# Optimization experiments

Hardware: AMD Instinct MI355X
Metric: run time of the kernel (lower is better)

The kernel has to match this reference:

```python
import jax, jax.numpy as jnp
import numpy as np

NUM_CLASSES = 26
IGNORE_LABEL = 0
LAMBDA_SMOOTH = 1.0
EPSILON = 1e-05
# static indices of valid (non-ignored) classes
_VALID = np.array([c for c in range(NUM_CLASSES) if c != IGNORE_LABEL])


def setup_inputs() -> dict:
    key = jax.random.key(0)
    k1, k2, k3 = jax.random.split(key, 3)
    B, D, H, W = 1, 160, 192, 224
    fixed_label_map = jax.random.randint(k1, (B, D, H, W), 0, NUM_CLASSES, dtype=jnp.int32)
    warped_moving_label_map = jax.random.randint(k2, (B, D, H, W), 0, NUM_CLASSES, dtype=jnp.int32)
    vector_field = jax.random.normal(k3, (B, 3, D, H, W), dtype=jnp.float32)
    return {
        'fixed_label_map': fixed_label_map,
        'warped_moving_label_map': warped_moving_label_map,
        'vector_field': vector_field,
    }


def _soft_dice(fixed, moving):
    # Equivalent to one-hot expansion + sum over (B,D,H,W), but computed
    # directly from integer labels via histogram counts (single pass).
    f = fixed.reshape(-1)
    m = moving.reshape(-1)
    fixed_vol = jnp.bincount(f, length=NUM_CLASSES).astype(jnp.float32)
    moving_vol = jnp.bincount(m, length=NUM_CLASSES).astype(jnp.float32)
    # intersection[c] = #{voxels: f==c and m==c}
    inter = jnp.bincount(f, weights=(f == m).astype(jnp.float32), length=NUM_CLASSES)
    dice = (2.0 * inter + EPSILON) / (fixed_vol + moving_vol + EPSILON)
    return 1.0 - dice[_VALID].mean()


def _diffusion(vf):
    # vf: [B, 3, D, H, W]
    dz = vf[:, :, 1:, :, :] - vf[:, :, :-1, :, :]
    dy = vf[:, :, :, 1:, :] - vf[:, :, :, :-1, :]
    dx = vf[:, :, :, :, 1:] - vf[:, :, :, :, :-1]
    return (jnp.mean(dz * dz) + jnp.mean(dy * dy) + jnp.mean(dx * dx)) / 3.0


def reference(fixed_label_map, warped_moving_label_map, vector_field):
    similarity_loss = _soft_dice(fixed_label_map, warped_moving_label_map)
    smoothness_loss = _diffusion(vector_field)
    total_loss = similarity_loss + LAMBDA_SMOOTH * smoothness_loss
    return (total_loss, similarity_loss, smoothness_loss)
```

## Files before the change

### kernel.cpp

```cpp
#include <hip/hip_runtime.h>


namespace {
constexpr int NC    = 26;
constexpr int Dd    = 160, Hh = 192, Ww = 224;
constexpr int W4    = Ww / 4;
constexpr int PL4   = Hh * W4;
constexpr int N4L   = Dd * Hh * Ww / 4;
constexpr int JSTRIDE = 33;
constexpr int NBINS   = NC * JSTRIDE;
constexpr int TPB     = 512;
constexpr int WPB     = TPB / 64;
constexpr int HIST_BLOCKS = 420;
constexpr int HT          = HIST_BLOCKS * TPB;
constexpr int SLAB    = 6;
constexpr int DCH     = 5;
constexpr int NTILES  = 3 * (Dd / DCH) * (Hh / SLAB);
constexpr int DIFF_WAVES  = NTILES / 2;
constexpr int DIFF_BLOCKS = DIFF_WAVES / WPB;
constexpr int FUSED_BLOCKS = DIFF_BLOCKS + HIST_BLOCKS;
}

__global__ void init_ws_kernel(unsigned int* __restrict__ joint,
                               double* __restrict__ sums) {
    int i = blockIdx.x * blockDim.x + threadIdx.x;
    if (i < NBINS) joint[i] = 0u;
    if (i < 3)     sums[i]  = 0.0;
}

__device__ __forceinline__ void hist_path(
        int hb,
        const int4* __restrict__ f4,
        const int4* __restrict__ m4,
        unsigned int* __restrict__ gj) {
    __shared__ unsigned int h[NBINS];
    for (int i = threadIdx.x; i < NBINS; i += TPB) h[i] = 0u;
    __syncthreads();

    const int g = hb * TPB + threadIdx.x;
    int4 a0 = f4[g];
    int4 a1 = f4[g + HT];
    int4 a2 = f4[g + 2 * HT];
    int4 a3 = f4[g + 3 * HT];
    int4 a4 = f4[g + 4 * HT];
    int4 a5 = f4[g + 5 * HT];
    int4 a6 = f4[g + 6 * HT];
    int4 a7 = f4[g + 7 * HT];
    int4 b0 = m4[g];
    int4 b1 = m4[g + HT];
    int4 b2 = m4[g + 2 * HT];
    int4 b3 = m4[g + 3 * HT];
    int4 b4 = m4[g + 4 * HT];
    int4 b5 = m4[g + 5 * HT];
    int4 b6 = m4[g + 6 * HT];
    int4 b7 = m4[g + 7 * HT];

#define JACC(A, B)                                   \
    atomicAdd(&h[(A).x * JSTRIDE + (B).x], 1u);      \
    atomicAdd(&h[(A).y * JSTRIDE + (B).y], 1u);      \
    atomicAdd(&h[(A).z * JSTRIDE + (B).z], 1u);      \
    atomicAdd(&h[(A).w * JSTRIDE + (B).w], 1u);
    JACC(a0, b0) JACC(a1, b1) JACC(a2, b2) JACC(a3, b3)
    JACC(a4, b4) JACC(a5, b5) JACC(a6, b6) JACC(a7, b7)
#undef JACC

    __syncthreads();
    for (int i = threadIdx.x; i < NBINS; i += TPB) {
        unsigned int v = h[i];
        if (v) atomicAdd(&gj[i], v);
    }
}

__device__ __forceinline__ void diff_path(
        int db,
        const float4* __restrict__ v4,
        double* __restrict__ gs) {
    const int lane = threadIdx.x & 63;
    const int wid  = threadIdx.x >> 6;
    const int w    = db * WPB + wid;
    const bool al  = (lane < W4);
    const int  l   = al ? lane : (W4 - 1);

    const int tA = w;
    const int cA = tA >> 10, remA = tA & 1023;
    const int d0A = (remA >> 5) * DCH;
    const int h0A = (remA & 31) * SLAB;
    const bool hvA = (h0A + SLAB < Hh);
    const int hOffA = (hvA ? SLAB : SLAB - 1) * W4;
    size_t curA = ((size_t)(cA * Dd + d0A) * Hh + h0A) * W4 + l;
    const int tB = w + DIFF_WAVES;
    const int cB = tB >> 10, remB = tB & 1023;
    const int d0B = (remB >> 5) * DCH;
    const int h0B = (remB & 31) * SLAB;
    const bool hvB = (h0B + SLAB < Hh);
    const int hOffB = (hvB ? SLAB : SLAB - 1) * W4;
    size_t curB = ((size_t)(cB * Dd + d0B) * Hh + h0B) * W4 + l;

    float4 pA0 = v4[curA];
    float4 pA1 = v4[curA + W4];
    float4 pA2 = v4[curA + 2 * W4];
    float4 pA3 = v4[curA + 3 * W4];
    float4 pA4 = v4[curA + 4 * W4];
    float4 pA5 = v4[curA + 5 * W4];
    float4 pB0 = v4[curB];
    float4 pB1 = v4[curB + W4];
    float4 pB2 = v4[curB + 2 * W4];
    float4 pB3 = v4[curB + 3 * W4];
    float4 pB4 = v4[curB + 4 * W4];
    float4 pB5 = v4[curB + 5 * W4];

    float sx = 0.f, sy = 0.f, sz = 0.f;

#define DX(P)                                                                  \
    {                                                                          \
        float d1 = (P).y - (P).x, d2 = (P).z - (P).y, d3 = (P).w - (P).z;      \
        sx += d1 * d1 + d2 * d2 + d3 * d3;                                     \
        float nx = __shfl_down((P).x, 1);                                      \
        float d4 = nx - (P).w;                                                 \
        sx += (lane < W4 - 1) ? d4 * d4 : 0.f;                                 \
    }
#define DY(A, B)                                                               \
    {                                                                          \
        float e0 = (B).x - (A).x, e1 = (B).y - (A).y;                          \
        float e2 = (B).z - (A).z, e3 = (B).w - (A).w;                          \
        sy += e0 * e0 + e1 * e1 + e2 * e2 + e3 * e3;                           \
    }
#define DZ(A, B)                                                               \
    {                                                                          \
        float e0 = (B).x - (A).x, e1 = (B).y - (A).y;                          \
        float e2 = (B).z - (A).z, e3 = (B).w - (A).w;                          \
        sz += e0 * e0 + e1 * e1 + e2 * e2 + e3 * e3;                           \
    }

    for (int k = 0; k < DCH; ++k) {
        const bool dzvA = (d0A + k < Dd - 1);
        const bool dzvB = (d0B + k < Dd - 1);
        float4 hlA = v4[curA + hOffA];
        float4 hlB = v4[curB + hOffB];
        float4 nA0 = pA0, nA1 = pA1, nA2 = pA2, nA3 = pA3, nA4 = pA4, nA5 = pA5;
        if (dzvA) {
            const size_t nb = curA + PL4;
            nA0 = v4[nb];
            nA1 = v4[nb + W4];
            nA2 = v4[nb + 2 * W4];
            nA3 = v4[nb + 3 * W4];
            nA4 = v4[nb + 4 * W4];
            nA5 = v4[nb + 5 * W4];
        }
        float4 nB0 = pB0, nB1 = pB1, nB2 = pB2, nB3 = pB3, nB4 = pB4, nB5 = pB5;
        if (dzvB) {
            const size_t nb = curB + PL4;
            nB0 = v4[nb];
            nB1 = v4[nb + W4];
            nB2 = v4[nb + 2 * W4];
            nB3 = v4[nb + 3 * W4];
            nB4 = v4[nb + 4 * W4];
            nB5 = v4[nb + 5 * W4];
        }

        DX(pA0) DX(pA1) DX(pA2) DX(pA3) DX(pA4) DX(pA5)
        DY(pA0, pA1) DY(pA1, pA2) DY(pA2, pA3) DY(pA3, pA4) DY(pA4, pA5)
        if (hvA) DY(pA5, hlA)
        if (dzvA) {
            DZ(pA0, nA0) DZ(pA1, nA1) DZ(pA2, nA2)
            DZ(pA3, nA3) DZ(pA4, nA4) DZ(pA5, nA5)
        }
        DX(pB0) DX(pB1) DX(pB2) DX(pB3) DX(pB4) DX(pB5)
        DY(pB0, pB1) DY(pB1, pB2) DY(pB2, pB3) DY(pB3, pB4) DY(pB4, pB5)
        if (hvB) DY(pB5, hlB)
        if (dzvB) {
            DZ(pB0, nB0) DZ(pB1, nB1) DZ(pB2, nB2)
            DZ(pB3, nB3) DZ(pB4, nB4) DZ(pB5, nB5)
        }

        pA0 = nA0; pA1 = nA1; pA2 = nA2; pA3 = nA3; pA4 = nA4; pA5 = nA5;
        pB0 = nB0; pB1 = nB1; pB2 = nB2; pB3 = nB3; pB4 = nB4; pB5 = nB5;
        curA += PL4; curB += PL4;
    }
#undef DX
#undef DY
#undef DZ

    if (!al) { sx = 0.f; sy = 0.f; sz = 0.f; }

    #pragma unroll
    for (int off = 32; off > 0; off >>= 1) {
        sx += __shfl_down(sx, off);
        sy += __shfl_down(sy, off);
        sz += __shfl_down(sz, off);
    }
    __shared__ float px[WPB], py[WPB], pz[WPB];
    if (lane == 0) { px[wid] = sx; py[wid] = sy; pz[wid] = sz; }
    __syncthreads();
    if (threadIdx.x == 0) {
        float tx = 0.f, ty = 0.f, tz = 0.f;
        #pragma unroll
        for (int i = 0; i < WPB; ++i) { tx += px[i]; ty += py[i]; tz += pz[i]; }
        atomicAdd(&gs[0], (double)tx);
        atomicAdd(&gs[1], (double)ty);
        atomicAdd(&gs[2], (double)tz);
    }
}

__global__ __launch_bounds__(512, 2) void fused_kernel(
        const int4* __restrict__ f4,
        const int4* __restrict__ m4,
        unsigned int* __restrict__ gj,
        const float4* __restrict__ v4,
        double* __restrict__ gs) {
    if (blockIdx.x < DIFF_BLOCKS) diff_path(blockIdx.x, v4, gs);
    else                          hist_path(blockIdx.x - DIFF_BLOCKS, f4, m4, gj);
}

__global__ void finalize_kernel(const unsigned int* __restrict__ gj,
                                const double* __restrict__ gs,
                                float* __restrict__ out) {
    int lane = threadIdx.x & 63;
    float term = 0.f;
    if (lane >= 1 && lane < NC) {
        float fv = 0.f, mv = 0.f;
        #pragma unroll
        for (int m = 0; m < NC; ++m) fv += (float)gj[lane * JSTRIDE + m];
        #pragma unroll
        for (int f = 0; f < NC; ++f) mv += (float)gj[f * JSTRIDE + lane];
        float iv = (float)gj[lane * JSTRIDE + lane];
        term = (2.f * iv + 1e-5f) / (fv + mv + 1e-5f);
    }
    #pragma unroll
    for (int off = 32; off > 0; off >>= 1) term += __shfl_down(term, off);
    if (threadIdx.x == 0 && blockIdx.x == 0) {
        float sim = 1.f - term * (1.f / 25.f);
        double mdx = gs[0] / ((double)3 * Dd * Hh * (Ww - 1));
        double mdy = gs[1] / ((double)3 * Dd * (Hh - 1) * Ww);
        double mdz = gs[2] / ((double)3 * (Dd - 1) * Hh * Ww);
        float smooth = (float)((mdx + mdy + mdz) / 3.0);
        out[0] = sim + smooth;
        out[1] = sim;
        out[2] = smooth;
    }
}

extern "C" void kernel_launch(void* const* d_in, const int* in_sizes, int n_in,
                              void* d_out, int out_size, void* d_ws, size_t ws_size,
                              hipStream_t stream) {
    const int*   fl = (const int*)d_in[0];
    const int*   ml = (const int*)d_in[1];
    const float* vf = (const float*)d_in[2];
    float* out = (float*)d_out;

    unsigned int* joint = (unsigned int*)d_ws;
    double*       sums  = (double*)((char*)d_ws + 3584);

    init_ws_kernel<<<1, 1024, 0, stream>>>(joint, sums);
    fused_kernel<<<FUSED_BLOCKS, TPB, 0, stream>>>(
        (const int4*)fl, (const int4*)ml, joint, (const float4*)vf, sums);
    finalize_kernel<<<1, 64, 0, stream>>>(joint, sums, out);
}
```

Measured before the change: 174.7 us.

## Replace global histogram atomics with per-block slots and drop the init kernel

When the workspace is large enough, each histogram block writes its private joint histogram into its own slot, and each diffusion block writes its partial sums into its own slot, with no global atomics. The finalize kernel then reduces all slots, so the init/zeroing launch is removed. The histogram grid shrinks to 105 blocks, each handling 4x more data. This trades global atomics and one launch for fewer, longer blocks and a heavier single-block finalize. If the workspace is too small, it falls back to the old path.

```diff
diff --git a/kernel.cpp b/kernel.cpp
--- a/kernel.cpp
+++ b/kernel.cpp
@@ -11,59 +11,77 @@
 constexpr int NBINS   = NC * JSTRIDE;
 constexpr int TPB     = 512;
 constexpr int WPB     = TPB / 64;
-constexpr int HIST_BLOCKS = 420;
-constexpr int HT          = HIST_BLOCKS * TPB;
+constexpr int HS_BLOCKS = 105;
+constexpr int HTS       = HS_BLOCKS * TPB;
+constexpr int HF_BLOCKS = 420;
+constexpr int HTF       = HF_BLOCKS * TPB;
 constexpr int SLAB    = 6;
 constexpr int DCH     = 5;
 constexpr int NTILES  = 3 * (Dd / DCH) * (Hh / SLAB);
 constexpr int DIFF_WAVES  = NTILES / 2;
 constexpr int DIFF_BLOCKS = DIFF_WAVES / WPB;
-constexpr int FUSED_BLOCKS = DIFF_BLOCKS + HIST_BLOCKS;
-}
-
-__global__ void init_ws_kernel(unsigned int* __restrict__ joint,
-                               double* __restrict__ sums) {
-    int i = blockIdx.x * blockDim.x + threadIdx.x;
-    if (i < NBINS) joint[i] = 0u;
-    if (i < 3)     sums[i]  = 0.0;
-}
-
-__device__ __forceinline__ void hist_path(
-        int hb,
-        const int4* __restrict__ f4,
-        const int4* __restrict__ m4,
-        unsigned int* __restrict__ gj) {
-    __shared__ unsigned int h[NBINS];
-    for (int i = threadIdx.x; i < NBINS; i += TPB) h[i] = 0u;
-    __syncthreads();
-
-    const int g = hb * TPB + threadIdx.x;
-    int4 a0 = f4[g];
-    int4 a1 = f4[g + HT];
-    int4 a2 = f4[g + 2 * HT];
-    int4 a3 = f4[g + 3 * HT];
-    int4 a4 = f4[g + 4 * HT];
-    int4 a5 = f4[g + 5 * HT];
-    int4 a6 = f4[g + 6 * HT];
-    int4 a7 = f4[g + 7 * HT];
-    int4 b0 = m4[g];
-    int4 b1 = m4[g + HT];
-    int4 b2 = m4[g + 2 * HT];
-    int4 b3 = m4[g + 3 * HT];
-    int4 b4 = m4[g + 4 * HT];
-    int4 b5 = m4[g + 5 * HT];
-    int4 b6 = m4[g + 6 * HT];
-    int4 b7 = m4[g + 7 * HT];
+constexpr int FS_BLOCKS = DIFF_BLOCKS + HS_BLOCKS;
+constexpr int FF_BLOCKS = DIFF_BLOCKS + HF_BLOCKS;
+constexpr size_t SLOT_BYTES = (size_t)HS_BLOCKS * NBINS * 4;
+constexpr size_t DPART_OFF  = 360448;
+constexpr size_t WS_NEEDED  = DPART_OFF + (size_t)DIFF_BLOCKS * 3 * 8;
+}
+
 
 #define JACC(A, B)                                   \
     atomicAdd(&h[(A).x * JSTRIDE + (B).x], 1u);      \
     atomicAdd(&h[(A).y * JSTRIDE + (B).y], 1u);      \
     atomicAdd(&h[(A).z * JSTRIDE + (B).z], 1u);      \
     atomicAdd(&h[(A).w * JSTRIDE + (B).w], 1u);
-    JACC(a0, b0) JACC(a1, b1) JACC(a2, b2) JACC(a3, b3)
+
+template <int HT>
+__device__ __forceinline__ void hist_step8(
+        unsigned int* h, const int4* __restrict__ f4,
+        const int4* __restrict__ m4, int b0) {
+    int4 a0 = f4[b0];
+    int4 a1 = f4[b0 + HT];
+    int4 a2 = f4[b0 + 2 * HT];
+    int4 a3 = f4[b0 + 3 * HT];
+    int4 a4 = f4[b0 + 4 * HT];
+    int4 a5 = f4[b0 + 5 * HT];
+    int4 a6 = f4[b0 + 6 * HT];
+    int4 a7 = f4[b0 + 7 * HT];
+    int4 b0v = m4[b0];
+    int4 b1 = m4[b0 + HT];
+    int4 b2 = m4[b0 + 2 * HT];
+    int4 b3 = m4[b0 + 3 * HT];
+    int4 b4 = m4[b0 + 4 * HT];
+    int4 b5 = m4[b0 + 5 * HT];
+    int4 b6 = m4[b0 + 6 * HT];
+    int4 b7 = m4[b0 + 7 * HT];
+    JACC(a0, b0v) JACC(a1, b1) JACC(a2, b2) JACC(a3, b3)
     JACC(a4, b4) JACC(a5, b5) JACC(a6, b6) JACC(a7, b7)
+}
 #undef JACC
 
+__device__ __forceinline__ void hist_slot(
+        int hb, const int4* __restrict__ f4, const int4* __restrict__ m4,
+        unsigned int* __restrict__ slots) {
+    __shared__ unsigned int h[NBINS];
+    for (int i = threadIdx.x; i < NBINS; i += TPB) h[i] = 0u;
+    __syncthreads();
+    const int g = hb * TPB + threadIdx.x;
+    #pragma unroll
+    for (int it = 0; it < 4; ++it)
+        hist_step8<HTS>(h, f4, m4, g + it * 8 * HTS);
+    __syncthreads();
+    unsigned int* slot = slots + (size_t)hb * NBINS;
+    for (int i = threadIdx.x; i < NBINS; i += TPB) slot[i] = h[i];
+}
+
+__device__ __forceinline__ void hist_atomic(
+        int hb, const int4* __restrict__ f4, const int4* __restrict__ m4,
+        unsigned int* __restrict__ gj) {
+    __shared__ unsigned int h[NBINS];
+    for (int i = threadIdx.x; i < NBINS; i += TPB) h[i] = 0u;
+    __syncthreads();
+    const int g = hb * TPB + threadIdx.x;
+    hist_step8<HTF>(h, f4, m4, g);
     __syncthreads();
     for (int i = threadIdx.x; i < NBINS; i += TPB) {
         unsigned int v = h[i];
@@ -71,10 +89,9 @@
     }
 }
 
+template <bool SLOT>
 __device__ __forceinline__ void diff_path(
-        int db,
-        const float4* __restrict__ v4,
-        double* __restrict__ gs) {
+        int db, const float4* __restrict__ v4, double* __restrict__ gs) {
     const int lane = threadIdx.x & 63;
     const int wid  = threadIdx.x >> 6;
     const int w    = db * WPB + wid;
@@ -196,10 +213,96 @@
         float tx = 0.f, ty = 0.f, tz = 0.f;
         #pragma unroll
         for (int i = 0; i < WPB; ++i) { tx += px[i]; ty += py[i]; tz += pz[i]; }
-        atomicAdd(&gs[0], (double)tx);
-        atomicAdd(&gs[1], (double)ty);
-        atomicAdd(&gs[2], (double)tz);
-    }
+        if constexpr (SLOT) {
+            gs[db * 3 + 0] = (double)tx;
+            gs[db * 3 + 1] = (double)ty;
+            gs[db * 3 + 2] = (double)tz;
+        } else {
+            atomicAdd(&gs[0], (double)tx);
+            atomicAdd(&gs[1], (double)ty);
+            atomicAdd(&gs[2], (double)tz);
+        }
+    }
+}
+
+
+__global__ __launch_bounds__(512, 2) void fused_slots_kernel(
+        const int4* __restrict__ f4,
+        const int4* __restrict__ m4,
+        unsigned int* __restrict__ slots,
+        const float4* __restrict__ v4,
+        double* __restrict__ dparts) {
+    if (blockIdx.x < DIFF_BLOCKS) diff_path<true>(blockIdx.x, v4, dparts);
+    else                          hist_slot(blockIdx.x - DIFF_BLOCKS, f4, m4, slots);
+}
+
+__global__ void finalize_slots_kernel(
+        const unsigned int* __restrict__ slots,
+        const double* __restrict__ dparts,
+        float* __restrict__ out) {
+    __shared__ unsigned int bins[NBINS];
+    __shared__ double wred[3][3];
+    const int t = threadIdx.x;
+
+    if (t < NBINS) {
+        unsigned int s = 0;
+        #pragma unroll 5
+        for (int b = 0; b < HS_BLOCKS; ++b) s += slots[(size_t)b * NBINS + t];
+        bins[t] = s;
+    }
+    double dx = 0.0, dy = 0.0, dz = 0.0;
+    if (t < DIFF_BLOCKS) {
+        dx = dparts[t * 3 + 0];
+        dy = dparts[t * 3 + 1];
+        dz = dparts[t * 3 + 2];
+    }
+    #pragma unroll
+    for (int off = 32; off > 0; off >>= 1) {
+        dx += __shfl_down(dx, off);
+        dy += __shfl_down(dy, off);
+        dz += __shfl_down(dz, off);
+    }
+    const int wv = t >> 6;
+    if ((t & 63) == 0 && wv < 3) {
+        wred[wv][0] = dx; wred[wv][1] = dy; wred[wv][2] = dz;
+    }
+    __syncthreads();
+
+    if (t < 64) {
+        float term = 0.f;
+        if (t >= 1 && t < NC) {
+            float fv = 0.f, mv = 0.f;
+            #pragma unroll
+            for (int m = 0; m < NC; ++m) fv += (float)bins[t * JSTRIDE + m];
+            #pragma unroll
+            for (int f = 0; f < NC; ++f) mv += (float)bins[f * JSTRIDE + t];
+            float iv = (float)bins[t * JSTRIDE + t];
+            term = (2.f * iv + 1e-5f) / (fv + mv + 1e-5f);
+        }
+        #pragma unroll
+        for (int off = 32; off > 0; off >>= 1) term += __shfl_down(term, off);
+        if (t == 0) {
+            double g0 = wred[0][0] + wred[1][0] + wred[2][0];
+            double g1 = wred[0][1] + wred[1][1] + wred[2][1];
+            double g2 = wred[0][2] + wred[1][2] + wred[2][2];
+            float sim = 1.f - term * (1.f / 25.f);
+            double mdx = g0 / ((double)3 * Dd * Hh * (Ww - 1));
+            double mdy = g1 / ((double)3 * Dd * (Hh - 1) * Ww);
+            double mdz = g2 / ((double)3 * (Dd - 1) * Hh * Ww);
+            float smooth = (float)((mdx + mdy + mdz) / 3.0);
+            out[0] = sim + smooth;
+            out[1] = sim;
+            out[2] = smooth;
+        }
+    }
+}
+
+
+__global__ void init_ws_kernel(unsigned int* __restrict__ joint,
+                               double* __restrict__ sums) {
+    int i = blockIdx.x * blockDim.x + threadIdx.x;
+    if (i < NBINS) joint[i] = 0u;
+    if (i < 3)     sums[i]  = 0.0;
 }
 
 __global__ __launch_bounds__(512, 2) void fused_kernel(
@@ -208,8 +311,8 @@
         unsigned int* __restrict__ gj,
         const float4* __restrict__ v4,
         double* __restrict__ gs) {
-    if (blockIdx.x < DIFF_BLOCKS) diff_path(blockIdx.x, v4, gs);
-    else                          hist_path(blockIdx.x - DIFF_BLOCKS, f4, m4, gj);
+    if (blockIdx.x < DIFF_BLOCKS) diff_path<false>(blockIdx.x, v4, gs);
+    else                          hist_atomic(blockIdx.x - DIFF_BLOCKS, f4, m4, gj);
 }
 
 __global__ void finalize_kernel(const unsigned int* __restrict__ gj,
@@ -240,6 +343,7 @@
     }
 }
 
+
 extern "C" void kernel_launch(void* const* d_in, const int* in_sizes, int n_in,
                               void* d_out, int out_size, void* d_ws, size_t ws_size,
                               hipStream_t stream) {
@@ -248,11 +352,18 @@
     const float* vf = (const float*)d_in[2];
     float* out = (float*)d_out;
 
-    unsigned int* joint = (unsigned int*)d_ws;
-    double*       sums  = (double*)((char*)d_ws + 3584);
-
-    init_ws_kernel<<<1, 1024, 0, stream>>>(joint, sums);
-    fused_kernel<<<FUSED_BLOCKS, TPB, 0, stream>>>(
-        (const int4*)fl, (const int4*)ml, joint, (const float4*)vf, sums);
-    finalize_kernel<<<1, 64, 0, stream>>>(joint, sums, out);
-}
+    if (ws_size >= WS_NEEDED) {
+        unsigned int* slots  = (unsigned int*)d_ws;
+        double*       dparts = (double*)((char*)d_ws + DPART_OFF);
+        fused_slots_kernel<<<FS_BLOCKS, TPB, 0, stream>>>(
+            (const int4*)fl, (const int4*)ml, slots, (const float4*)vf, dparts);
+        finalize_slots_kernel<<<1, 1024, 0, stream>>>(slots, dparts, out);
+    } else {
+        unsigned int* joint = (unsigned int*)d_ws;
+        double*       sums  = (double*)((char*)d_ws + 3584);
+        init_ws_kernel<<<1, 1024, 0, stream>>>(joint, sums);
+        fused_kernel<<<FF_BLOCKS, TPB, 0, stream>>>(
+            (const int4*)fl, (const int4*)ml, joint, (const float4*)vf, sums);
+        finalize_kernel<<<1, 64, 0, stream>>>(joint, sums, out);
+    }
+}
```

Result: slower. 188.4 us (+7.9%).
